# Kernel optimization log

Hardware: AMD Instinct MI355X
Metric: run time of the kernel (lower is better)

## Reference

```python
import jax, jax.numpy as jnp
import numpy as np

D_MODEL = 1024
E_MODEL = 2
D_STATE = 16
D_CONV = 4
D_IN = E_MODEL * D_MODEL            # 2048
DT_RANK = int(np.ceil(D_MODEL / 16))  # 64
B_SZ, SEQ = 1, 2048


def setup_inputs() -> dict:
    key = jax.random.key(0)
    ks = jax.random.split(key, 9)
    s = lambda fan: 1.0 / np.sqrt(fan)
    return {
        "x": jax.random.normal(ks[0], (B_SZ, SEQ, D_MODEL), jnp.float32),
        "W_in": jax.random.normal(ks[1], (D_MODEL, 2 * D_IN), jnp.float32) * s(D_MODEL),
        "conv_w": jax.random.normal(ks[2], (D_CONV, D_IN), jnp.float32) * s(D_CONV),
        "conv_b": jnp.zeros((D_IN,), jnp.float32),
        "W_x": jax.random.normal(ks[3], (D_IN, DT_RANK + 2 * D_STATE), jnp.float32) * s(D_IN),
        "W_dt": jax.random.normal(ks[4], (DT_RANK, D_IN), jnp.float32) * s(DT_RANK),
        "b_dt": jax.random.normal(ks[5], (D_IN,), jnp.float32) * 0.01,
        "D": jnp.ones((D_IN,), jnp.float32),
        "W_out": jax.random.normal(ks[6], (D_IN, D_MODEL), jnp.float32) * s(D_IN),
    }


def _causal_depthwise_conv(x, w, b):
    # x: (b, l, d_in); w: (d_conv, d_in) depthwise taps; causal left pad
    L = x.shape[1]
    xp = jnp.pad(x, ((0, 0), (D_CONV - 1, 0), (0, 0)))
    y = b
    for k in range(D_CONV):  # small fixed kernel width
        y = y + xp[:, k:k + L, :] * w[k]
    return y


def _selective_scan(u, delta, A, Bm, Cm, D):
    # u, delta: (b,l,d); A: (d,n); Bm, Cm: (b,l,n); D: (d,)
    dA = jnp.einsum('bld,dn->bldn', delta, A)
    dB_u = jnp.einsum('bld,bld,bln->bldn', delta, u, Bm)
    # replicate tf.pad(dA[:,1:], [[0,0],[1,1],[0,0],[0,0]])[:,1:]
    t = jnp.pad(dA[:, 1:], ((0, 0), (1, 1), (0, 0), (0, 0)))[:, 1:]
    t = jnp.flip(t, axis=1)
    t = jnp.cumsum(t, axis=1)
    dA_cs = jnp.flip(jnp.exp(t), axis=1)
    xs = jnp.cumsum(dB_u * dA_cs, axis=1) / (dA_cs + 1e-12)
    y = jnp.einsum('bldn,bln->bld', xs, Cm)
    return y + u * D


def reference(x, W_in, conv_w, conv_b, W_x, W_dt, b_dt, D, W_out):
    seq_len = x.shape[1]
    x_and_res = x @ W_in                                  # (b,l,2*d_in)
    xi, res = jnp.split(x_and_res, [D_IN], axis=-1)
    xi = _causal_depthwise_conv(xi, conv_w, conv_b)[:, :seq_len, :]
    xi = jax.nn.swish(xi)
    # SSM
    A = -jnp.exp(jnp.log(jnp.arange(1, D_STATE + 1, dtype=jnp.float32)))  # (n,)
    A = jnp.broadcast_to(A, (D_IN, D_STATE))
    x_dbl = xi @ W_x                                      # (b,l,dtr+2n)
    delta, Bm, Cm = jnp.split(x_dbl, [DT_RANK, DT_RANK + D_STATE], axis=-1)
    delta = jax.nn.softplus(delta @ W_dt + b_dt)          # (b,l,d_in)
    y = _selective_scan(xi, delta, A, Bm, Cm, D)
    y = y * jax.nn.swish(res)
    return y @ W_out
```

## Files before the change

kernel.cpp:

```cpp
#include <hip/hip_runtime.h>
#include <hip/hip_bf16.h>

#define L_SEQ 2048
#define DMODEL 1024
#define DIN 2048
#define DTR 64
#define NST 16
#define CCH 128
#define CHL 16

typedef unsigned short u16;
typedef __bf16 bf16x8 __attribute__((ext_vector_type(8)));
typedef float f32x4 __attribute__((ext_vector_type(4)));

__device__ inline u16 f2bf(float v) {
    __bf16 h = (__bf16)v;
    return __builtin_bit_cast(unsigned short, h);
}
__device__ inline float bf2f(u16 v) {
    __bf16 h = __builtin_bit_cast(__bf16, v);
    return (float)h;
}
__device__ inline float rcpf(float x) { return __builtin_amdgcn_rcpf(x); }
__device__ inline float swishf(float v) { return v * rcpf(1.f + __expf(-v)); }
__device__ inline float softplusf(float v) {
    return (v > 20.f) ? v : __logf(1.f + __expf(v));
}

__device__ inline void powers16(float v, float* p) {
    p[0] = v;
    p[1] = v * v;
    p[2] = p[1] * v;
    p[3] = p[1] * p[1];
    p[4] = p[3] * p[0];  p[5] = p[3] * p[1];  p[6] = p[3] * p[2];  p[7] = p[3] * p[3];
    p[8] = p[7] * p[0];  p[9] = p[7] * p[1];  p[10] = p[7] * p[2]; p[11] = p[7] * p[3];
    p[12] = p[7] * p[4]; p[13] = p[7] * p[5]; p[14] = p[7] * p[6]; p[15] = p[7] * p[7];
}

template<int TBN, int EPI>
__global__ __launch_bounds__(256) void gemm_bf16(const u16* __restrict__ A,
                                                 const u16* __restrict__ Bt,
                                                 float* __restrict__ C,
                                                 const float* __restrict__ bias,
                                                 u16* __restrict__ xiraw,
                                                 float* __restrict__ gate,
                                                 int M, int N, int K) {
    constexpr int LDSZ = (128 + TBN) * 64;
    constexpr int ROUNDS = (128 + TBN) / 32;
    constexpr int FN = TBN / 32;
    __shared__ u16 smem[2 * LDSZ];

    const int tid = threadIdx.x;
    const int lane = tid & 63;
    const int wid = tid >> 6;
    const int wm = wid >> 1;
    const int wn = wid & 1;
    const int bm = blockIdx.y * 128;
    const int bn = blockIdx.x * TBN;

    const int srow8 = lane >> 3;
    const int schunk = lane & 7;
    const int sgchunk = schunk ^ srow8;
    const int lm = lane & 15;
    const int lk = lane >> 4;

    f32x4 acc[4][FN];
#pragma unroll
    for (int i = 0; i < 4; ++i)
#pragma unroll
        for (int j = 0; j < FN; ++j) acc[i][j] = (f32x4){0.f, 0.f, 0.f, 0.f};

    auto stage = [&](int buf, int t) {
        const int k0 = t * 64;
        u16* base = smem + buf * LDSZ;
#pragma unroll
        for (int rr = 0; rr < ROUNDS; ++rr) {
            int row = rr * 32 + wid * 8;
            int grow = row + srow8;
            const u16* src;
            if (row < 128) src = A + (size_t)(bm + grow) * K + k0 + sgchunk * 8;
            else           src = Bt + (size_t)(bn + grow - 128) * K + k0 + sgchunk * 8;
            u16* dst = base + row * 64;
            __builtin_amdgcn_global_load_lds(
                (const __attribute__((address_space(1))) void*)src,
                (__attribute__((address_space(3))) void*)dst, 16, 0, 0);
        }
    };

    auto compute = [&](int buf) {
        const u16* base = smem + buf * LDSZ;
#pragma unroll
        for (int kk = 0; kk < 2; ++kk) {
            bf16x8 av[4], bv[FN];
#pragma unroll
            for (int fm = 0; fm < 4; ++fm) {
                int row = wm * 64 + fm * 16 + lm;
                int slot = (kk * 4 + lk) ^ (row & 7);
                av[fm] = *(const bf16x8*)(base + row * 64 + slot * 8);
            }
#pragma unroll
            for (int fn = 0; fn < FN; ++fn) {
                int row = 128 + wn * (TBN / 2) + fn * 16 + lm;
                int slot = (kk * 4 + lk) ^ (row & 7);
                bv[fn] = *(const bf16x8*)(base + row * 64 + slot * 8);
            }
#pragma unroll
            for (int fm = 0; fm < 4; ++fm)
#pragma unroll
                for (int fn = 0; fn < FN; ++fn)
                    acc[fm][fn] = __builtin_amdgcn_mfma_f32_16x16x32_bf16(av[fm], bv[fn], acc[fm][fn], 0, 0, 0);
        }
    };

    const int nt = K / 64;
    int cur = 0;
    stage(0, 0);
    for (int t = 0; t < nt - 1; ++t) {
        stage(cur ^ 1, t + 1);
        asm volatile("s_waitcnt vmcnt(%0) lgkmcnt(0)\n\ts_barrier"
                     :: "n"(ROUNDS) : "memory");
        compute(cur);
        asm volatile("s_waitcnt lgkmcnt(0)\n\ts_barrier" ::: "memory");
        cur ^= 1;
    }
    asm volatile("s_waitcnt vmcnt(0) lgkmcnt(0)\n\ts_barrier" ::: "memory");
    compute(cur);

#pragma unroll
    for (int fm = 0; fm < 4; ++fm) {
#pragma unroll
        for (int fn = 0; fn < FN; ++fn) {
            int col = bn + wn * (TBN / 2) + fn * 16 + lm;
#pragma unroll
            for (int j = 0; j < 4; ++j) {
                int row = bm + wm * 64 + fm * 16 + lk * 4 + j;
                float v = acc[fm][fn][j];
                if (EPI == 0) {
                    C[(size_t)row * N + col] = v;
                } else if (EPI == 1) {
                    v += bias[col];
                    C[(size_t)row * N + col] = softplusf(v);
                } else {
                    if (col < DIN) xiraw[(size_t)row * DIN + col] = f2bf(v);
                    else           gate[(size_t)row * DIN + (col - DIN)] = swishf(v);
                }
            }
        }
    }
}

__global__ __launch_bounds__(256) void gemm_bf16_sk(const u16* __restrict__ A, int lda,
                                                    const u16* __restrict__ Bt, int ldb,
                                                    float* __restrict__ P,
                                                    int M, int N, int K, int kc) {
    constexpr int TBN = 32;
    constexpr int LDSZ = (128 + TBN) * 64;
    constexpr int ROUNDS = (128 + TBN) / 32;
    __shared__ u16 smem[2 * LDSZ];

    const int tid = threadIdx.x;
    const int lane = tid & 63;
    const int wid = tid >> 6;
    const int wm = wid >> 1;
    const int wn = wid & 1;
    const int bm = blockIdx.y * 128;
    const int bn = blockIdx.x * TBN;
    const int kbeg = blockIdx.z * kc;
    float* Cz = P + (size_t)blockIdx.z * M * N;

    const int srow8 = lane >> 3;
    const int schunk = lane & 7;
    const int sgchunk = schunk ^ srow8;
    const int lm = lane & 15;
    const int lk = lane >> 4;

    f32x4 acc[4];
#pragma unroll
    for (int i = 0; i < 4; ++i) acc[i] = (f32x4){0.f, 0.f, 0.f, 0.f};

    auto stage = [&](int buf, int t) {
        const int k0 = kbeg + t * 64;
        u16* base = smem + buf * LDSZ;
#pragma unroll
        for (int rr = 0; rr < ROUNDS; ++rr) {
            int row = rr * 32 + wid * 8;
            int grow = row + srow8;
            const u16* src;
            if (row < 128) src = A + (size_t)(bm + grow) * lda + k0 + sgchunk * 8;
            else           src = Bt + (size_t)(bn + grow - 128) * ldb + k0 + sgchunk * 8;
            u16* dst = base + row * 64;
            __builtin_amdgcn_global_load_lds(
                (const __attribute__((address_space(1))) void*)src,
                (__attribute__((address_space(3))) void*)dst, 16, 0, 0);
        }
    };

    auto compute = [&](int buf) {
        const u16* base = smem + buf * LDSZ;
#pragma unroll
        for (int kk = 0; kk < 2; ++kk) {
            bf16x8 av[4], bv;
#pragma unroll
            for (int fm = 0; fm < 4; ++fm) {
                int row = wm * 64 + fm * 16 + lm;
                int slot = (kk * 4 + lk) ^ (row & 7);
                av[fm] = *(const bf16x8*)(base + row * 64 + slot * 8);
            }
            {
                int row = 128 + wn * 16 + lm;
                int slot = (kk * 4 + lk) ^ (row & 7);
                bv = *(const bf16x8*)(base + row * 64 + slot * 8);
            }
#pragma unroll
            for (int fm = 0; fm < 4; ++fm)
                acc[fm] = __builtin_amdgcn_mfma_f32_16x16x32_bf16(av[fm], bv, acc[fm], 0, 0, 0);
        }
    };

    const int nt = kc / 64;
    int cur = 0;
    stage(0, 0);
    for (int t = 0; t < nt - 1; ++t) {
        stage(cur ^ 1, t + 1);
        asm volatile("s_waitcnt vmcnt(%0) lgkmcnt(0)\n\ts_barrier"
                     :: "n"(ROUNDS) : "memory");
        compute(cur);
        asm volatile("s_waitcnt lgkmcnt(0)\n\ts_barrier" ::: "memory");
        cur ^= 1;
    }
    asm volatile("s_waitcnt vmcnt(0) lgkmcnt(0)\n\ts_barrier" ::: "memory");
    compute(cur);

#pragma unroll
    for (int fm = 0; fm < 4; ++fm) {
        int col = bn + wn * 16 + lm;
#pragma unroll
        for (int j = 0; j < 4; ++j) {
            int row = bm + wm * 64 + fm * 16 + lk * 4 + j;
            Cz[(size_t)row * N + col] = acc[fm][j];
        }
    }
}

__device__ inline void castT_dev(const float* __restrict__ W, u16* __restrict__ Wt,
                                 int K, int N, int bx, int by) {
    __shared__ u16 tile[64][65];
    int n0 = bx * 64, k0 = by * 64;
    int tn = threadIdx.x & 63, t4 = threadIdx.x >> 6;
#pragma unroll
    for (int j = 0; j < 16; ++j) {
        int k = t4 + j * 4;
        if (n0 + tn < N) tile[tn][k] = f2bf(W[(size_t)(k0 + k) * N + n0 + tn]);
    }
    __syncthreads();
#pragma unroll
    for (int j = 0; j < 16; ++j) {
        int n = t4 + j * 4;
        if (n0 + n < N) Wt[(size_t)(n0 + n) * K + k0 + tn] = tile[n][tn];
    }
}

__global__ __launch_bounds__(256) void prep_fused(const float* __restrict__ x,
                                                  const float* __restrict__ W_in,
                                                  const float* __restrict__ W_x,
                                                  const float* __restrict__ W_dt,
                                                  const float* __restrict__ W_out,
                                                  u16* __restrict__ xbf,
                                                  u16* __restrict__ WinT,
                                                  u16* __restrict__ WxT,
                                                  u16* __restrict__ WdtT,
                                                  u16* __restrict__ WoutT) {
    int b = blockIdx.x;
    if (b < 2048) {
        int i = b * 256 + threadIdx.x;
        float4 v = ((const float4*)x)[i];
        ushort4 o;
        o.x = f2bf(v.x); o.y = f2bf(v.y); o.z = f2bf(v.z); o.w = f2bf(v.w);
        ((ushort4*)xbf)[i] = o;
    } else if (b < 3072) {
        int t = b - 2048;
        castT_dev(W_in, WinT, DMODEL, 4096, t & 63, t >> 6);
    } else if (b < 3136) {
        int t = b - 3072;
        castT_dev(W_x, WxT, DIN, 96, t & 1, t >> 1);
    } else if (b < 3168) {
        int t = b - 3136;
        castT_dev(W_dt, WdtT, DTR, DIN, t, 0);
    } else {
        int t = b - 3168;
        castT_dev(W_out, WoutT, DIN, DMODEL, t & 15, t >> 4);
    }
}

__global__ __launch_bounds__(256) void reduce_sk(const float* __restrict__ P,
                                                 float* __restrict__ xdbl,
                                                 u16* __restrict__ xdbf) {
    int i = blockIdx.x * 256 + threadIdx.x;
    float s = 0.f;
#pragma unroll
    for (int z = 0; z < 4; ++z) s += P[z * (L_SEQ * 96) + i];
    xdbl[i] = s;
    int l = i / 96, k = i - l * 96;
    if (k < DTR) xdbf[l * DTR + k] = f2bf(s);
}

__global__ __launch_bounds__(256) void conv_swish(const u16* __restrict__ xiraw,
                                                  const float* __restrict__ cw,
                                                  const float* __restrict__ cb,
                                                  u16* __restrict__ xib) {
    int id = blockIdx.x * 256 + threadIdx.x;
    int l = id >> 11;
    int d = id & (DIN - 1);
    float acc = cb[d];
#pragma unroll
    for (int k = 0; k < 4; ++k) {
        int ls = l - 3 + k;
        if (ls >= 0) acc += bf2f(xiraw[ls * DIN + d]) * cw[k * DIN + d];
    }
    xib[id] = f2bf(swishf(acc));
}

__global__ __launch_bounds__(256) void scanA(const float* __restrict__ delta,
                                             const u16* __restrict__ u,
                                             const float* __restrict__ xdbl,
                                             float* __restrict__ localQ,
                                             float* __restrict__ csum) {
    __shared__ float sh[CHL][16];
    const int tid = threadIdx.x;
    const int c = blockIdx.y;
    const int d = blockIdx.x * 256 + tid;
    const int l0 = c * CHL;
    {
        int l = tid >> 4, j = tid & 15;
        sh[l][j] = xdbl[(l0 + l) * 96 + DTR + j];
    }
    __syncthreads();
    float q[16];
#pragma unroll
    for (int n = 0; n < 16; ++n) q[n] = 0.f;
    float s = 0.f;
#pragma unroll 2
    for (int l = 0; l < CHL; ++l) {
        float dl = delta[(l0 + l) * DIN + d];
        float ul = bf2f(u[(l0 + l) * DIN + d]);
        float bb[16];
        const float4* shv = (const float4*)&sh[l][0];
        *(float4*)&bb[0] = shv[0];  *(float4*)&bb[4] = shv[1];
        *(float4*)&bb[8] = shv[2];  *(float4*)&bb[12] = shv[3];
        float v = __expf(-dl);
        float p[16];
        powers16(v, p);
        float dlul = dl * ul;
#pragma unroll
        for (int n = 0; n < 16; ++n) q[n] = q[n] * p[n] + dlul * bb[n];
        s += dl;
    }
    float* dst = localQ + (size_t)(c * DIN + d) * 16;
    *(float4*)(dst + 0)  = make_float4(q[0], q[1], q[2], q[3]);
    *(float4*)(dst + 4)  = make_float4(q[4], q[5], q[6], q[7]);
    *(float4*)(dst + 8)  = make_float4(q[8], q[9], q[10], q[11]);
    *(float4*)(dst + 12) = make_float4(q[12], q[13], q[14], q[15]);
    csum[c * DIN + d] = s;
}

__global__ __launch_bounds__(256) void scanB(float* __restrict__ localQ,
                                             const float* __restrict__ csum,
                                             float* __restrict__ send) {
    int gid = blockIdx.x * 256 + threadIdx.x;
    int n = gid & 15;
    int d = gid >> 4;
    const float An = -(float)(n + 1);
    float q = 0.f;
#pragma unroll 4
    for (int c = 0; c < CCH; ++c) {
        float cs = csum[c * DIN + d];
        float w = __expf(An * cs);
        float* lq = localQ + (size_t)(c * DIN + d) * 16 + n;
        float lv = *lq;
        *lq = q;
        q = q * w + lv;
    }
    if (n == 0) {
        double ssum = 0.0;
        for (int c = CCH - 1; c >= 0; --c) {
            ssum += (double)csum[c * DIN + d];
            send[c * DIN + d] = (float)ssum;
        }
    }
}

__global__ __launch_bounds__(256) void scanC(const float* __restrict__ delta,
                                             const u16* __restrict__ u,
                                             const float* __restrict__ xdbl,
                                             const float* __restrict__ localQ,
                                             const float* __restrict__ send,
                                             const float* __restrict__ Dvec,
                                             const float* __restrict__ gate,
                                             u16* __restrict__ ybf) {
    __shared__ float sh[CHL][32];
    const int tid = threadIdx.x;
    const int c = blockIdx.y;
    const int d = blockIdx.x * 256 + tid;
    const int l0 = c * CHL;
#pragma unroll
    for (int k = 0; k < 2; ++k) {
        int idx = tid + k * 256;
        int l = idx >> 5, j = idx & 31;
        sh[l][j] = xdbl[(l0 + l) * 96 + DTR + j];
    }
    __syncthreads();
    float q[16];
    {
        const float* src = localQ + (size_t)(c * DIN + d) * 16;
        float4 t0 = *(const float4*)(src + 0);
        float4 t1 = *(const float4*)(src + 4);
        float4 t2 = *(const float4*)(src + 8);
        float4 t3 = *(const float4*)(src + 12);
        q[0] = t0.x; q[1] = t0.y; q[2] = t0.z; q[3] = t0.w;
        q[4] = t1.x; q[5] = t1.y; q[6] = t1.z; q[7] = t1.w;
        q[8] = t2.x; q[9] = t2.y; q[10] = t2.z; q[11] = t2.w;
        q[12] = t3.x; q[13] = t3.y; q[14] = t3.z; q[15] = t3.w;
    }
    const float send_cd = send[c * DIN + d];
    const float Dd = Dvec[d];
    float s = 0.f;
#pragma unroll 2
    for (int l = 0; l < CHL; ++l) {
        float dl = delta[(l0 + l) * DIN + d];
        float ul = bf2f(u[(l0 + l) * DIN + d]);
        float bb[32];
        const float4* shv = (const float4*)&sh[l][0];
        *(float4*)&bb[0]  = shv[0]; *(float4*)&bb[4]  = shv[1];
        *(float4*)&bb[8]  = shv[2]; *(float4*)&bb[12] = shv[3];
        *(float4*)&bb[16] = shv[4]; *(float4*)&bb[20] = shv[5];
        *(float4*)&bb[24] = shv[6]; *(float4*)&bb[28] = shv[7];
        float v = __expf(-dl);
        float p[16];
        powers16(v, p);
        float dlul = dl * ul;
#pragma unroll
        for (int n = 0; n < 16; ++n) q[n] = q[n] * p[n] + dlul * bb[n];
        s += dl;
        float suf = send_cd - s;
        float contrib;
        float ac[4] = {0.f, 0.f, 0.f, 0.f};
        if (suf < 0.8f) {
#pragma unroll
            for (int n = 0; n < 16; ++n) ac[n & 3] += q[n] * bb[16 + n];
            contrib = (ac[0] + ac[1]) + (ac[2] + ac[3]);
        } else {
            float w = __expf(-suf);
            float e[16];
            powers16(w, e);
            if (suf > 40.f) {
#pragma unroll
                for (int n = 0; n < 16; ++n) ac[n & 3] += (q[n] * e[n]) * bb[16 + n];
                contrib = ((ac[0] + ac[1]) + (ac[2] + ac[3])) * 1e12f;
            } else {
#pragma unroll
                for (int n = 0; n < 16; ++n) {
                    float g = e[n] * rcpf(e[n] + 1e-12f);
                    ac[n & 3] += (q[n] * g) * bb[16 + n];
                }
                contrib = (ac[0] + ac[1]) + (ac[2] + ac[3]);
            }
        }
        float y = contrib + ul * Dd;
        ybf[(l0 + l) * DIN + d] = f2bf(y * gate[(l0 + l) * DIN + d]);
    }
}

extern "C" void kernel_launch(void* const* d_in, const int* in_sizes, int n_in,
                              void* d_out, int out_size, void* d_ws, size_t ws_size,
                              hipStream_t stream) {
    const float* x      = (const float*)d_in[0];
    const float* W_in   = (const float*)d_in[1];
    const float* conv_w = (const float*)d_in[2];
    const float* conv_b = (const float*)d_in[3];
    const float* W_x    = (const float*)d_in[4];
    const float* W_dt   = (const float*)d_in[5];
    const float* b_dt   = (const float*)d_in[6];
    const float* Dvec   = (const float*)d_in[7];
    const float* W_out  = (const float*)d_in[8];
    float* out = (float*)d_out;

    float* ws = (float*)d_ws;
    u16*   xiraw  = (u16*)ws;
    float* gate   = ws + 2097152;
    u16*   xibf   = (u16*)(ws + 6291456);
    float* xdbl   = ws + 8388608;
    float* delta  = ws + 8585216;
    float* localQ = ws + 12779520;
    float* csum   = ws + 16973824;
    float* send   = ws + 17235968;
    u16*   xbf    = (u16*)(ws + 17498112);
    u16*   WinT   = (u16*)(ws + 18546688);
    u16*   WxT    = (u16*)(ws + 20643840);
    u16*   WdtT   = (u16*)(ws + 20742144);
    u16*   WoutT  = (u16*)(ws + 20807680);
    u16*   xdbf   = (u16*)(ws + 21856256);
    float* Psk    = ws + 21921792;
    u16*   ybf    = (u16*)(ws + 22708224);

    prep_fused<<<3680, 256, 0, stream>>>(x, W_in, W_x, W_dt, W_out,
                                         xbf, WinT, WxT, WdtT, WoutT);
    gemm_bf16<64, 2><<<dim3(4096 / 64, L_SEQ / 128), 256, 0, stream>>>(
        xbf, WinT, nullptr, nullptr, xiraw, gate, L_SEQ, 4096, DMODEL);
    conv_swish<<<(L_SEQ * DIN) / 256, 256, 0, stream>>>(xiraw, conv_w, conv_b, xibf);
    gemm_bf16_sk<<<dim3(3, L_SEQ / 128, 4), 256, 0, stream>>>(
        xibf, DIN, WxT, DIN, Psk, L_SEQ, 96, DIN, 512);
    reduce_sk<<<(L_SEQ * 96) / 256, 256, 0, stream>>>(Psk, xdbl, xdbf);
    gemm_bf16<64, 1><<<dim3(DIN / 64, L_SEQ / 128), 256, 0, stream>>>(
        xdbf, WdtT, delta, b_dt, nullptr, nullptr, L_SEQ, DIN, DTR);
    scanA<<<dim3(DIN / 256, CCH), 256, 0, stream>>>(delta, xibf, xdbl, localQ, csum);
    scanB<<<(DIN * NST) / 256, 256, 0, stream>>>(localQ, csum, send);
    scanC<<<dim3(DIN / 256, CCH), 256, 0, stream>>>(delta, xibf, xdbl, localQ, send,
                                                    Dvec, gate, ybf);
    gemm_bf16<32, 0><<<dim3(DMODEL / 32, L_SEQ / 128), 256, 0, stream>>>(
        ybf, WoutT, out, nullptr, nullptr, nullptr, L_SEQ, DMODEL, DIN);
}
```

Measured before the change: 151.8 us.

## Store delta transposed and preload per-chunk delta and u in scan kernels

The delta GEMM epilogue now writes softplus output in a transposed (d, L) layout using float4 stores along the sequence axis. scanA and scanC use that layout to load each thread's 16 chunk deltas with four float4 loads, preload the 16 u values into registers up front, and unroll the time loop by 4. The aim is to take global loads out of the serial recurrence and give the scan more independent work per step. In exchange, the GEMM epilogue stores and the per-lane delta reads become strided across lanes instead of coalesced, and register pressure rises.

```diff
diff --git a/kernel.cpp b/kernel.cpp
--- a/kernel.cpp
+++ b/kernel.cpp
@@ -131,18 +131,26 @@
 #pragma unroll
         for (int fn = 0; fn < FN; ++fn) {
             int col = bn + wn * (TBN / 2) + fn * 16 + lm;
-#pragma unroll
-            for (int j = 0; j < 4; ++j) {
-                int row = bm + wm * 64 + fm * 16 + lk * 4 + j;
-                float v = acc[fm][fn][j];
-                if (EPI == 0) {
-                    C[(size_t)row * N + col] = v;
-                } else if (EPI == 1) {
-                    v += bias[col];
-                    C[(size_t)row * N + col] = softplusf(v);
-                } else {
-                    if (col < DIN) xiraw[(size_t)row * DIN + col] = f2bf(v);
-                    else           gate[(size_t)row * DIN + (col - DIN)] = swishf(v);
+            if (EPI == 1) {
+                float b = bias[col];
+                float4 o;
+                o.x = softplusf(acc[fm][fn][0] + b);
+                o.y = softplusf(acc[fm][fn][1] + b);
+                o.z = softplusf(acc[fm][fn][2] + b);
+                o.w = softplusf(acc[fm][fn][3] + b);
+                int rowb = bm + wm * 64 + fm * 16 + lk * 4;
+                *(float4*)(C + (size_t)col * M + rowb) = o;
+            } else {
+#pragma unroll
+                for (int j = 0; j < 4; ++j) {
+                    int row = bm + wm * 64 + fm * 16 + lk * 4 + j;
+                    float v = acc[fm][fn][j];
+                    if (EPI == 0) {
+                        C[(size_t)row * N + col] = v;
+                    } else {
+                        if (col < DIN) xiraw[(size_t)row * DIN + col] = f2bf(v);
+                        else           gate[(size_t)row * DIN + (col - DIN)] = swishf(v);
+                    }
                 }
             }
         }
@@ -320,7 +328,7 @@
     xib[id] = f2bf(swishf(acc));
 }
 
-__global__ __launch_bounds__(256) void scanA(const float* __restrict__ delta,
+__global__ __launch_bounds__(256) void scanA(const float* __restrict__ deltaT,
                                              const u16* __restrict__ u,
                                              const float* __restrict__ xdbl,
                                              float* __restrict__ localQ,
@@ -335,25 +343,38 @@
         sh[l][j] = xdbl[(l0 + l) * 96 + DTR + j];
     }
     __syncthreads();
+    float dl[CHL];
+    {
+        const float4* dp = (const float4*)(deltaT + (size_t)d * L_SEQ + l0);
+        float4 v0 = dp[0], v1 = dp[1], v2 = dp[2], v3 = dp[3];
+        dl[0] = v0.x; dl[1] = v0.y; dl[2] = v0.z; dl[3] = v0.w;
+        dl[4] = v1.x; dl[5] = v1.y; dl[6] = v1.z; dl[7] = v1.w;
+        dl[8] = v2.x; dl[9] = v2.y; dl[10] = v2.z; dl[11] = v2.w;
+        dl[12] = v3.x; dl[13] = v3.y; dl[14] = v3.z; dl[15] = v3.w;
+    }
+    u16 uls[CHL];
+#pragma unroll
+    for (int l = 0; l < CHL; ++l) uls[l] = u[(l0 + l) * DIN + d];
+
     float q[16];
 #pragma unroll
     for (int n = 0; n < 16; ++n) q[n] = 0.f;
     float s = 0.f;
-#pragma unroll 2
+#pragma unroll 4
     for (int l = 0; l < CHL; ++l) {
-        float dl = delta[(l0 + l) * DIN + d];
-        float ul = bf2f(u[(l0 + l) * DIN + d]);
+        float dlv = dl[l];
+        float ulv = bf2f(uls[l]);
         float bb[16];
         const float4* shv = (const float4*)&sh[l][0];
         *(float4*)&bb[0] = shv[0];  *(float4*)&bb[4] = shv[1];
         *(float4*)&bb[8] = shv[2];  *(float4*)&bb[12] = shv[3];
-        float v = __expf(-dl);
+        float v = __expf(-dlv);
         float p[16];
         powers16(v, p);
-        float dlul = dl * ul;
+        float dlul = dlv * ulv;
 #pragma unroll
         for (int n = 0; n < 16; ++n) q[n] = q[n] * p[n] + dlul * bb[n];
-        s += dl;
+        s += dlv;
     }
     float* dst = localQ + (size_t)(c * DIN + d) * 16;
     *(float4*)(dst + 0)  = make_float4(q[0], q[1], q[2], q[3]);
@@ -389,7 +410,7 @@
     }
 }
 
-__global__ __launch_bounds__(256) void scanC(const float* __restrict__ delta,
+__global__ __launch_bounds__(256) void scanC(const float* __restrict__ deltaT,
                                              const u16* __restrict__ u,
                                              const float* __restrict__ xdbl,
                                              const float* __restrict__ localQ,
@@ -409,6 +430,19 @@
         sh[l][j] = xdbl[(l0 + l) * 96 + DTR + j];
     }
     __syncthreads();
+    float dl[CHL];
+    {
+        const float4* dp = (const float4*)(deltaT + (size_t)d * L_SEQ + l0);
+        float4 v0 = dp[0], v1 = dp[1], v2 = dp[2], v3 = dp[3];
+        dl[0] = v0.x; dl[1] = v0.y; dl[2] = v0.z; dl[3] = v0.w;
+        dl[4] = v1.x; dl[5] = v1.y; dl[6] = v1.z; dl[7] = v1.w;
+        dl[8] = v2.x; dl[9] = v2.y; dl[10] = v2.z; dl[11] = v2.w;
+        dl[12] = v3.x; dl[13] = v3.y; dl[14] = v3.z; dl[15] = v3.w;
+    }
+    u16 uls[CHL];
+#pragma unroll
+    for (int l = 0; l < CHL; ++l) uls[l] = u[(l0 + l) * DIN + d];
+
     float q[16];
     {
         const float* src = localQ + (size_t)(c * DIN + d) * 16;
@@ -424,23 +458,23 @@
     const float send_cd = send[c * DIN + d];
     const float Dd = Dvec[d];
     float s = 0.f;
-#pragma unroll 2
+#pragma unroll 4
     for (int l = 0; l < CHL; ++l) {
-        float dl = delta[(l0 + l) * DIN + d];
-        float ul = bf2f(u[(l0 + l) * DIN + d]);
+        float dlv = dl[l];
+        float ulv = bf2f(uls[l]);
         float bb[32];
         const float4* shv = (const float4*)&sh[l][0];
         *(float4*)&bb[0]  = shv[0]; *(float4*)&bb[4]  = shv[1];
         *(float4*)&bb[8]  = shv[2]; *(float4*)&bb[12] = shv[3];
         *(float4*)&bb[16] = shv[4]; *(float4*)&bb[20] = shv[5];
         *(float4*)&bb[24] = shv[6]; *(float4*)&bb[28] = shv[7];
-        float v = __expf(-dl);
+        float v = __expf(-dlv);
         float p[16];
         powers16(v, p);
-        float dlul = dl * ul;
+        float dlul = dlv * ulv;
 #pragma unroll
         for (int n = 0; n < 16; ++n) q[n] = q[n] * p[n] + dlul * bb[n];
-        s += dl;
+        s += dlv;
         float suf = send_cd - s;
         float contrib;
         float ac[4] = {0.f, 0.f, 0.f, 0.f};
@@ -465,7 +499,7 @@
                 contrib = (ac[0] + ac[1]) + (ac[2] + ac[3]);
             }
         }
-        float y = contrib + ul * Dd;
+        float y = contrib + ulv * Dd;
         ybf[(l0 + l) * DIN + d] = f2bf(y * gate[(l0 + l) * DIN + d]);
     }
 }
@@ -489,7 +523,7 @@
     float* gate   = ws + 2097152;
     u16*   xibf   = (u16*)(ws + 6291456);
     float* xdbl   = ws + 8388608;
-    float* delta  = ws + 8585216;
+    float* deltaT = ws + 8585216;
     float* localQ = ws + 12779520;
     float* csum   = ws + 16973824;
     float* send   = ws + 17235968;
@@ -511,10 +545,10 @@
         xibf, DIN, WxT, DIN, Psk, L_SEQ, 96, DIN, 512);
     reduce_sk<<<(L_SEQ * 96) / 256, 256, 0, stream>>>(Psk, xdbl, xdbf);
     gemm_bf16<64, 1><<<dim3(DIN / 64, L_SEQ / 128), 256, 0, stream>>>(
-        xdbf, WdtT, delta, b_dt, nullptr, nullptr, L_SEQ, DIN, DTR);
-    scanA<<<dim3(DIN / 256, CCH), 256, 0, stream>>>(delta, xibf, xdbl, localQ, csum);
+        xdbf, WdtT, deltaT, b_dt, nullptr, nullptr, L_SEQ, DIN, DTR);
+    scanA<<<dim3(DIN / 256, CCH), 256, 0, stream>>>(deltaT, xibf, xdbl, localQ, csum);
     scanB<<<(DIN * NST) / 256, 256, 0, stream>>>(localQ, csum, send);
-    scanC<<<dim3(DIN / 256, CCH), 256, 0, stream>>>(delta, xibf, xdbl, localQ, send,
+    scanC<<<dim3(DIN / 256, CCH), 256, 0, stream>>>(deltaT, xibf, xdbl, localQ, send,
                                                     Dvec, gate, ybf);
     gemm_bf16<32, 0><<<dim3(DMODEL / 32, L_SEQ / 128), 256, 0, stream>>>(
         ybf, WoutT, out, nullptr, nullptr, nullptr, L_SEQ, DMODEL, DIN);
```

After: 154.7 us. About the same (+1.9%).
